# Kernel tuning notes

Measured on AMD Instinct MI355X. Metric: run time of the kernel, lower is better.

Reference implementation:

```python
import jax, jax.numpy as jnp
import numpy as np

B, S, E = 256, 500, 128
NUM_Q, NUM_C, DL = 10000, 1000, 100


def _linear_params(key, fan_in, fan_out):
    kw, kb = jax.random.split(key)
    W = jax.random.normal(kw, (fan_out, fan_in), jnp.float32) * 0.02
    b = jnp.zeros((fan_out,), jnp.float32)
    return W, b


def setup_inputs() -> dict:
    key = jax.random.key(0)
    ks = jax.random.split(key, 24)
    W1, b1 = _linear_params(ks[0], 4 * E, E)
    W2, b2 = _linear_params(ks[1], E, E)
    W3, b3 = _linear_params(ks[2], E, E)
    W4, b4 = _linear_params(ks[3], 2 * E, E)
    W5, b5 = _linear_params(ks[4], 2 * E, E)
    W6, b6 = _linear_params(ks[5], 4 * E, E)
    inp = {
        'q': jax.random.randint(ks[6], (B, S), 0, NUM_Q + 1, dtype=jnp.int32),
        'c': jax.random.randint(ks[7], (B, S), 0, NUM_C + 1, dtype=jnp.int32),
        'sd': jax.random.randint(ks[8], (B, S), 0, DL + 2, dtype=jnp.int32),
        'qd': jax.random.randint(ks[9], (B, S), 0, DL + 2, dtype=jnp.int32),
        'a': jax.random.randint(ks[10], (B, S), 0, 2, dtype=jnp.int32),
        'qshft': jax.random.randint(ks[11], (B, S), 0, NUM_Q + 1, dtype=jnp.int32),
        'cshft': jax.random.randint(ks[12], (B, S), 0, NUM_C + 1, dtype=jnp.int32),
        'sdshft': jax.random.randint(ks[13], (B, S), 0, DL + 2, dtype=jnp.int32),
        'qdshft': jax.random.randint(ks[14], (B, S), 0, DL + 2, dtype=jnp.int32),
        'q_embedding': jax.random.normal(ks[15], (B, S, E), jnp.float32),
        'c_tab': jax.random.normal(ks[16], (NUM_C + 1, E), jnp.float32) * 0.02,
        'sd_tab': jax.random.normal(ks[17], (DL + 2, E), jnp.float32) * 0.02,
        'qd_tab': jax.random.normal(ks[18], (DL + 2, E), jnp.float32) * 0.02,
        'a_tab': jax.random.normal(ks[19], (2, E), jnp.float32) * 0.02,
        'knowledge': jax.random.normal(ks[20], (1, E), jnp.float32) * 0.1,
        'W1': W1, 'b1': b1, 'W2': W2, 'b2': b2, 'W3': W3, 'b3': b3,
        'W4': W4, 'b4': b4, 'W5': W5, 'b5': b5, 'W6': W6, 'b6': b6,
    }
    return inp


def reference(q, c, sd, qd, a, qshft, cshft, sdshft, qdshft, q_embedding,
              c_tab, sd_tab, qd_tab, a_tab, knowledge,
              W1, b1, W2, b2, W3, b3, W4, b4, W5, b5, W6, b6):
    # padding_idx=0 embeddings -> zero row 0
    mask0 = lambda t: t.at[0].set(0.0)
    c_e = mask0(c_tab)[c]      # [B,S,E]
    sd_e = mask0(sd_tab)[sd]   # [B,S,E]
    qd_e = mask0(qd_tab)[qd]   # [B,S,E]
    a_e = a_tab[a]             # [B,S,E]
    # linear_1 on concatenated (q, c, sd, qd) embeddings
    input_data = jnp.concatenate([q_embedding, c_e, sd_e, qd_e], -1) @ W1.T + b1  # [B,S,E]
    # time-major for scan
    xs = (jnp.swapaxes(input_data, 0, 1), jnp.swapaxes(a_e, 0, 1),
          jnp.swapaxes(sd_e, 0, 1), jnp.swapaxes(qd_e, 0, 1))
    k0 = jnp.broadcast_to(knowledge, (q.shape[0], knowledge.shape[1]))  # [B,E]

    def step(k, x):
        inp_t, a_t, sd_t, qd_t = x
        qq = k - inp_t
        g_sdf = jax.nn.sigmoid(qq @ W2.T + b2)
        sdft = g_sdf * jnp.tanh(qq @ W3.T + b3)      # dropout in eval mode = identity
        xcat = jnp.concatenate([sdft, a_t], -1)
        g_pka = jax.nn.sigmoid(xcat @ W4.T + b4)
        pkat = g_pka * jnp.tanh(xcat @ W5.T + b5)
        ins = jnp.concatenate([k, a_t, sd_t, qd_t], -1)
        g_ksu = jax.nn.sigmoid(ins @ W6.T + b6)
        k_new = g_ksu * k + (1.0 - g_ksu) * pkat
        return k_new, None

    k_final, _ = jax.lax.scan(step, k0, xs)
    return jax.nn.sigmoid(k_final)  # [B,E]
```

## Files before the change

kernel.cpp:

```cpp
#include <hip/hip_runtime.h>

typedef unsigned short u16;
typedef unsigned int u32;
typedef short bf16x8 __attribute__((ext_vector_type(8)));
typedef float f32x4 __attribute__((ext_vector_type(4)));

#define S_LEN 500
#define NB 256
#define EDIM 128

__device__ __forceinline__ float bf2f(u16 u) { return __uint_as_float(((u32)u) << 16); }
__device__ __forceinline__ u16 f2bf(float f) {
    u32 x = __float_as_uint(f);
    x += 0x7FFFu + ((x >> 16) & 1u);
    return (u16)(x >> 16);
}
__device__ __forceinline__ u32 cvtpk(float lo, float hi) {
    u32 r;
    asm("v_cvt_pk_bf16_f32 %0, %1, %2" : "=v"(r) : "v"(lo), "v"(hi));
    return r;
}
__device__ __forceinline__ float fexp(float x) { return __builtin_amdgcn_exp2f(x * 1.44269504089f); }
__device__ __forceinline__ float frcp(float x) { return __builtin_amdgcn_rcpf(x); }
__device__ __forceinline__ float sigm(float x) { return frcp(1.0f + fexp(-x)); }
__device__ __forceinline__ float tanh_(float x) { return 1.0f - 2.0f * frcp(1.0f + fexp(2.0f * x)); }
__device__ __forceinline__ int iclamp(int v, int hi) { return v < 0 ? 0 : (v > hi ? hi : v); }

__device__ __forceinline__ void wgsync(volatile int* c, int target) {
    __asm__ volatile("s_waitcnt lgkmcnt(0)" ::: "memory");
    if ((threadIdx.x & 63) == 0) atomicAdd((int*)c, 1);
    while (*c < target) {}
    __asm__ volatile("" ::: "memory");
}

__device__ __forceinline__ bool detect_bf16(const void* q) {
    const u16* w = (const u16*)q;
    int plaus = 0;
#pragma unroll 1
    for (int i = 0; i < 64; ++i) {
        const u16 v = w[2 * i];
        const int e = (v >> 7) & 0xFF;
        plaus += (v == 0 || (e >= 100 && e <= 130)) ? 1 : 0;
    }
    return plaus >= 48;
}
__device__ __forceinline__ float ldF(const void* p, int i, bool bf) {
    return bf ? bf2f(((const u16*)p)[i]) : ((const float*)p)[i];
}
template <bool BF>
__device__ __forceinline__ bf16x8 ldfragT(const void* p, int i) {
    if (BF) return *(const bf16x8*)((const u16*)p + i);
    const float* f = (const float*)p + i;
    bf16x8 r;
#pragma unroll
    for (int e = 0; e < 8; ++e) r[e] = (short)f2bf(f[e]);
    return r;
}
__device__ __forceinline__ bf16x8 ldfragR(const void* p, int i, bool bf) {
    if (bf) return *(const bf16x8*)((const u16*)p + i);
    const float* f = (const float*)p + i;
    bf16x8 r;
#pragma unroll
    for (int e = 0; e < 8; ++e) r[e] = (short)f2bf(f[e]);
    return r;
}

__global__ void dimkt_sentinel(u16* __restrict__ out, u16 val) {
    out[blockIdx.x * 256 + threadIdx.x] = val;
}

__global__ void dimkt_qe16(const float* __restrict__ qf, u16* __restrict__ qe16) {
    if (detect_bf16(qf)) return;
    const int i = (blockIdx.x * 256 + threadIdx.x) * 8;
    const float4 a = *(const float4*)(qf + i);
    const float4 b = *(const float4*)(qf + i + 4);
    ushort4 lo, hi;
    lo.x = f2bf(a.x); lo.y = f2bf(a.y); lo.z = f2bf(a.z); lo.w = f2bf(a.w);
    hi.x = f2bf(b.x); hi.y = f2bf(b.y); hi.z = f2bf(b.z); hi.w = f2bf(b.w);
    *(ushort4*)(qe16 + i) = lo;
    *(ushort4*)(qe16 + i + 4) = hi;
}

__global__ void dimkt_w1bf(const void* __restrict__ W1, const void* __restrict__ qref,
                           u16* __restrict__ W1b) {
    const bool bf = detect_bf16(qref);
    const int i = blockIdx.x * 256 + threadIdx.x;
    W1b[i] = bf ? ((const u16*)W1)[i] : f2bf(((const float*)W1)[i]);
}

__global__ void dimkt_tabs(const void* __restrict__ q_emb,
                           const void* __restrict__ c_tab, const void* __restrict__ sd_tab,
                           const void* __restrict__ qd_tab, const void* __restrict__ a_tab,
                           const void* __restrict__ W1, const void* __restrict__ W4,
                           const void* __restrict__ W5, const void* __restrict__ W6,
                           const void* __restrict__ b4, const void* __restrict__ b5,
                           const void* __restrict__ b6,
                           float* __restrict__ cW1p, float* __restrict__ sdQ,
                           float* __restrict__ qdQ, float* __restrict__ aW6p,
                           float* __restrict__ c4t, float* __restrict__ c5t) {
    const bool bf = detect_bf16(q_emb);
    __shared__ float src[128];
    const int r = blockIdx.x, n = threadIdx.x;
    const void* srcp; const void* W; const void* bias = nullptr;
    int soff, koff, ld, oidx; float* outp; bool mask;
    if (r < 1001)      { srcp = c_tab;  soff = r * 128;               W = W1; koff = 128; ld = 512; outp = cW1p; oidx = r * 128 + n;           mask = (r == 0); }
    else if (r < 1103) { int rr = r - 1001; srcp = sd_tab; soff = rr * 128; W = W1; koff = 256; ld = 512; outp = sdQ;  oidx = rr * 256 + n * 2;     mask = (rr == 0); }
    else if (r < 1205) { int rr = r - 1103; srcp = qd_tab; soff = rr * 128; W = W1; koff = 384; ld = 512; outp = qdQ;  oidx = rr * 256 + n * 2;     mask = (rr == 0); }
    else if (r < 1307) { int rr = r - 1205; srcp = sd_tab; soff = rr * 128; W = W6; koff = 256; ld = 512; outp = sdQ;  oidx = rr * 256 + n * 2 + 1; mask = (rr == 0); }
    else if (r < 1409) { int rr = r - 1307; srcp = qd_tab; soff = rr * 128; W = W6; koff = 384; ld = 512; outp = qdQ;  oidx = rr * 256 + n * 2 + 1; mask = (rr == 0); }
    else if (r < 1411) { int rr = r - 1409; srcp = a_tab;  soff = rr * 128; W = W6; koff = 128; ld = 512; outp = aW6p; oidx = rr * 128 + n;         bias = b6; mask = false; }
    else if (r < 1413) { int rr = r - 1411; srcp = a_tab;  soff = rr * 128; W = W4; koff = 128; ld = 256; outp = c4t;  oidx = rr * 128 + n;         bias = b4; mask = false; }
    else               { int rr = r - 1413; srcp = a_tab;  soff = rr * 128; W = W5; koff = 128; ld = 256; outp = c5t;  oidx = rr * 128 + n;         bias = b5; mask = false; }
    src[n] = ldF(srcp, soff + n, bf);
    __syncthreads();
    float acc = 0.f;
    if (!mask) {
        if (bf) {
            const u16* Wp = (const u16*)W + n * ld + koff;
#pragma unroll 4
            for (int k = 0; k < 128; k += 8) {
                const ushort4 wa = *(const ushort4*)(Wp + k);
                const ushort4 wb = *(const ushort4*)(Wp + k + 4);
                acc += src[k] * bf2f(wa.x) + src[k + 1] * bf2f(wa.y)
                     + src[k + 2] * bf2f(wa.z) + src[k + 3] * bf2f(wa.w)
                     + src[k + 4] * bf2f(wb.x) + src[k + 5] * bf2f(wb.y)
                     + src[k + 6] * bf2f(wb.z) + src[k + 7] * bf2f(wb.w);
            }
        } else {
            const float* Wp = (const float*)W + n * ld + koff;
#pragma unroll 4
            for (int k = 0; k < 128; k += 4) {
                const float4 w4 = *(const float4*)(Wp + k);
                acc += src[k] * w4.x + src[k + 1] * w4.y + src[k + 2] * w4.z + src[k + 3] * w4.w;
            }
        }
        if (bias) acc += ldF(bias, n, bf);
    }
    outp[oidx] = acc;
}

__global__ void dimkt_inp(const void* __restrict__ q_emb, const u16* __restrict__ qe16,
                          const u16* __restrict__ W1b, const int fastpath,
                          const void* __restrict__ W1, const void* __restrict__ b1,
                          const int* __restrict__ cI, const int* __restrict__ sI,
                          const int* __restrict__ qI, const int* __restrict__ aI,
                          const float* __restrict__ cW1p, const float* __restrict__ sdQ,
                          const float* __restrict__ qdQ, const float* __restrict__ aW6p,
                          u16* __restrict__ INP16, u32* __restrict__ INPZ6T, const int pk) {
    const bool bf = detect_bf16(q_emb);
    const int t = blockIdx.x, rc = blockIdx.y;
    const int lane = threadIdx.x, quad = lane >> 4, l15 = lane & 15;
    const bool fA = bf || (fastpath != 0);
    const u16* aes = bf ? (const u16*)q_emb : qe16;
    bf16x8 ae[4];
#pragma unroll
    for (int ks = 0; ks < 4; ++ks) {
        const int off = ((rc * 16 + l15) * S_LEN + t) * EDIM + ks * 32 + quad * 8;
        ae[ks] = fA ? *(const bf16x8*)(aes + off) : ldfragR(q_emb, off, false);
    }
    int cx[4], sx[4], qx[4], ax[4];
#pragma unroll
    for (int i = 0; i < 4; ++i) {
        const int off = (rc * 16 + quad * 4 + i) * S_LEN + t;
        cx[i] = iclamp(cI[off], 1000);
        sx[i] = iclamp(sI[off], 101);
        qx[i] = iclamp(qI[off], 101);
        ax[i] = iclamp(aI[off], 1);
    }
#pragma unroll 1
    for (int ct = 0; ct < 8; ++ct) {
        const int colc = ct * 16 + l15;
        bf16x8 w[4];
#pragma unroll
        for (int ks = 0; ks < 4; ++ks) {
            const int woff = colc * 512 + ks * 32 + quad * 8;
            w[ks] = fastpath ? *(const bf16x8*)(W1b + woff) : ldfragR(W1, woff, bf);
        }
        const float b1c = ldF(b1, colc, bf);
        f32x4 acc; float z6v[4];
#pragma unroll
        for (int i = 0; i < 4; ++i) {
            const float2 sgp = *(const float2*)(sdQ + sx[i] * 256 + colc * 2);
            const float2 qgp = *(const float2*)(qdQ + qx[i] * 256 + colc * 2);
            acc[i] = b1c + cW1p[cx[i] * 128 + colc] + sgp.x + qgp.x;
            z6v[i] = pk ? (aW6p[ax[i] * 128 + colc] + sgp.y + qgp.y) : 0.f;
        }
#pragma unroll
        for (int ks = 0; ks < 4; ++ks)
            acc = __builtin_amdgcn_mfma_f32_16x16x32_bf16(ae[ks], w[ks], acc, 0, 0, 0);
        if (pk) {
            uint4 st;
            st.x = cvtpk(acc[0], z6v[0]); st.y = cvtpk(acc[1], z6v[1]);
            st.z = cvtpk(acc[2], z6v[2]); st.w = cvtpk(acc[3], z6v[3]);
            *(uint4*)(INPZ6T + ((size_t)t * 128 + colc) * 256 + rc * 16 + quad * 4) = st;
        } else {
#pragma unroll
            for (int i = 0; i < 4; ++i)
                INP16[((size_t)t * 256 + rc * 16 + quad * 4 + i) * 128 + colc] = f2bf(acc[i]);
        }
    }
}

template <bool BF>
__global__ __launch_bounds__(512, 2) void dimkt_scan_pk(
    const void* __restrict__ q_emb, const u32* __restrict__ INPZ6T,
    const int* __restrict__ aI,
    const void* __restrict__ W2, const void* __restrict__ b2,
    const void* __restrict__ W3, const void* __restrict__ b3,
    const void* __restrict__ W4, const void* __restrict__ W5,
    const void* __restrict__ W6, const void* __restrict__ knowledge,
    const float* __restrict__ c4t, const float* __restrict__ c5t,
    void* __restrict__ outv) {
    if (detect_bf16(q_emb) != BF) return;
    __shared__ __align__(16) u16 kbuf[16][136];
    __shared__ __align__(16) u16 qqbuf[16][136];
    __shared__ __align__(16) u16 sdbuf[16][136];
    __shared__ int sctr;

    const int tid = threadIdx.x;
    const int wv = tid >> 6, lane = tid & 63;
    const int quad = lane >> 4, l15 = lane & 15;
    const int b0 = blockIdx.x * 16;
    const int col = wv * 16 + l15;

    bf16x8 fW2[4], fW3[4], fW4[4], fW5[4], fW6[4];
#pragma unroll
    for (int ks = 0; ks < 4; ++ks) {
        const int ko = ks * 32 + quad * 8;
        fW2[ks] = ldfragT<BF>(W2, col * 128 + ko);
        fW3[ks] = ldfragT<BF>(W3, col * 128 + ko);
        fW4[ks] = ldfragT<BF>(W4, col * 256 + ko);
        fW5[ks] = ldfragT<BF>(W5, col * 256 + ko);
        fW6[ks] = ldfragT<BF>(W6, col * 512 + ko);
    }
    const float b2v = ldF(b2, col, BF);
    const float b3v = ldF(b3, col, BF);
    const float c4_0 = c4t[col], c4_1 = c4t[128 + col];
    const float c5_0 = c5t[col], c5_1 = c5t[128 + col];

    const u32* pzBase = INPZ6T + (size_t)col * 256 + b0 + quad * 4;
    const int aRow = (b0 + quad * 4) * S_LEN;

    float kold[4], z6c[4], g[4];
    int ac[4];
    {
        const float k0 = ldF(knowledge, col, BF);
        const u16 k0b = f2bf(k0);
        const uint4 pz0 = *(const uint4*)pzBase;
        const u32 pzv[4] = {pz0.x, pz0.y, pz0.z, pz0.w};
        if (tid == 0) sctr = 0;
#pragma unroll
        for (int i = 0; i < 4; ++i) {
            ac[i] = iclamp(aI[aRow + i * S_LEN], 1);
            z6c[i] = __uint_as_float(pzv[i] & 0xFFFF0000u);
            const float inp0 = __uint_as_float(pzv[i] << 16);
            kold[i] = k0;
            kbuf[quad * 4 + i][col] = k0b;
            qqbuf[quad * 4 + i][col] = f2bf(k0 - inp0);
        }
    }
    __syncthreads();

    int bar = 0;
#pragma unroll 1
    for (int t = 0; t < S_LEN; ++t) {
        const int tp = (t + 1 < S_LEN) ? t + 1 : S_LEN - 1;
        int an[4];
#pragma unroll
        for (int i = 0; i < 4; ++i) an[i] = iclamp(aI[aRow + i * S_LEN + tp], 1);
        const uint4 pzN = *(const uint4*)(pzBase + (size_t)tp * 32768);

        bf16x8 aq[4], ak[4];
#pragma unroll
        for (int ks = 0; ks < 4; ++ks) {
            aq[ks] = *(const bf16x8*)&qqbuf[l15][ks * 32 + quad * 8];
            ak[ks] = *(const bf16x8*)&kbuf[l15][ks * 32 + quad * 8];
        }
        f32x4 Y2a = (f32x4){b2v, b2v, b2v, b2v}, Y2b = (f32x4){0.f, 0.f, 0.f, 0.f};
        f32x4 Y3a = (f32x4){b3v, b3v, b3v, b3v}, Y3b = (f32x4){0.f, 0.f, 0.f, 0.f};
        f32x4 Y6a = (f32x4){z6c[0], z6c[1], z6c[2], z6c[3]}, Y6b = (f32x4){0.f, 0.f, 0.f, 0.f};
        Y2a = __builtin_amdgcn_mfma_f32_16x16x32_bf16(aq[0], fW2[0], Y2a, 0, 0, 0);
        Y3a = __builtin_amdgcn_mfma_f32_16x16x32_bf16(aq[0], fW3[0], Y3a, 0, 0, 0);
        Y6a = __builtin_amdgcn_mfma_f32_16x16x32_bf16(ak[0], fW6[0], Y6a, 0, 0, 0);
        Y2b = __builtin_amdgcn_mfma_f32_16x16x32_bf16(aq[2], fW2[2], Y2b, 0, 0, 0);
        Y3b = __builtin_amdgcn_mfma_f32_16x16x32_bf16(aq[2], fW3[2], Y3b, 0, 0, 0);
        Y6b = __builtin_amdgcn_mfma_f32_16x16x32_bf16(ak[2], fW6[2], Y6b, 0, 0, 0);
        Y2a = __builtin_amdgcn_mfma_f32_16x16x32_bf16(aq[1], fW2[1], Y2a, 0, 0, 0);
        Y3a = __builtin_amdgcn_mfma_f32_16x16x32_bf16(aq[1], fW3[1], Y3a, 0, 0, 0);
        Y6a = __builtin_amdgcn_mfma_f32_16x16x32_bf16(ak[1], fW6[1], Y6a, 0, 0, 0);
        Y2b = __builtin_amdgcn_mfma_f32_16x16x32_bf16(aq[3], fW2[3], Y2b, 0, 0, 0);
        Y3b = __builtin_amdgcn_mfma_f32_16x16x32_bf16(aq[3], fW3[3], Y3b, 0, 0, 0);
        Y6b = __builtin_amdgcn_mfma_f32_16x16x32_bf16(ak[3], fW6[3], Y6b, 0, 0, 0);
        const f32x4 Y2 = Y2a + Y2b, Y3 = Y3a + Y3b, Y6 = Y6a + Y6b;
        float sdv[4];
#pragma unroll
        for (int i = 0; i < 4; ++i) sdv[i] = sigm(Y2[i]) * tanh_(Y3[i]);
        {
            const u32 s01 = cvtpk(sdv[0], sdv[1]), s23 = cvtpk(sdv[2], sdv[3]);
            sdbuf[quad * 4 + 0][col] = (u16)s01;
            sdbuf[quad * 4 + 1][col] = (u16)(s01 >> 16);
            sdbuf[quad * 4 + 2][col] = (u16)s23;
            sdbuf[quad * 4 + 3][col] = (u16)(s23 >> 16);
        }
        bar += 8; wgsync(&sctr, bar);

        bf16x8 as[4];
#pragma unroll
        for (int ks = 0; ks < 4; ++ks)
            as[ks] = *(const bf16x8*)&sdbuf[l15][ks * 32 + quad * 8];
#pragma unroll
        for (int i = 0; i < 4; ++i) g[i] = sigm(Y6[i]);
        f32x4 Y4a = (f32x4){ac[0] ? c4_1 : c4_0, ac[1] ? c4_1 : c4_0,
                            ac[2] ? c4_1 : c4_0, ac[3] ? c4_1 : c4_0};
        f32x4 Y5a = (f32x4){ac[0] ? c5_1 : c5_0, ac[1] ? c5_1 : c5_0,
                            ac[2] ? c5_1 : c5_0, ac[3] ? c5_1 : c5_0};
        f32x4 Y4b = (f32x4){0.f, 0.f, 0.f, 0.f}, Y5b = (f32x4){0.f, 0.f, 0.f, 0.f};
        Y4a = __builtin_amdgcn_mfma_f32_16x16x32_bf16(as[0], fW4[0], Y4a, 0, 0, 0);
        Y5a = __builtin_amdgcn_mfma_f32_16x16x32_bf16(as[0], fW5[0], Y5a, 0, 0, 0);
        Y4b = __builtin_amdgcn_mfma_f32_16x16x32_bf16(as[2], fW4[2], Y4b, 0, 0, 0);
        Y5b = __builtin_amdgcn_mfma_f32_16x16x32_bf16(as[2], fW5[2], Y5b, 0, 0, 0);
        Y4a = __builtin_amdgcn_mfma_f32_16x16x32_bf16(as[1], fW4[1], Y4a, 0, 0, 0);
        Y5a = __builtin_amdgcn_mfma_f32_16x16x32_bf16(as[1], fW5[1], Y5a, 0, 0, 0);
        Y4b = __builtin_amdgcn_mfma_f32_16x16x32_bf16(as[3], fW4[3], Y4b, 0, 0, 0);
        Y5b = __builtin_amdgcn_mfma_f32_16x16x32_bf16(as[3], fW5[3], Y5b, 0, 0, 0);
        const f32x4 Y4 = Y4a + Y4b, Y5 = Y5a + Y5b;
        const u32 pzv[4] = {pzN.x, pzN.y, pzN.z, pzN.w};
        float knA[4], qqA[4];
#pragma unroll
        for (int i = 0; i < 4; ++i) {
            const float pk = sigm(Y4[i]) * tanh_(Y5[i]);
            const float kn = g[i] * kold[i] + (1.0f - g[i]) * pk;
            kold[i] = kn; knA[i] = kn;
            qqA[i] = kn - __uint_as_float(pzv[i] << 16);
        }
        {
            const u32 k01 = cvtpk(knA[0], knA[1]), k23 = cvtpk(knA[2], knA[3]);
            const u32 q01 = cvtpk(qqA[0], qqA[1]), q23 = cvtpk(qqA[2], qqA[3]);
            kbuf[quad * 4 + 0][col] = (u16)k01;
            kbuf[quad * 4 + 1][col] = (u16)(k01 >> 16);
            kbuf[quad * 4 + 2][col] = (u16)k23;
            kbuf[quad * 4 + 3][col] = (u16)(k23 >> 16);
            qqbuf[quad * 4 + 0][col] = (u16)q01;
            qqbuf[quad * 4 + 1][col] = (u16)(q01 >> 16);
            qqbuf[quad * 4 + 2][col] = (u16)q23;
            qqbuf[quad * 4 + 3][col] = (u16)(q23 >> 16);
        }
#pragma unroll
        for (int i = 0; i < 4; ++i) {
            z6c[i] = __uint_as_float(pzv[i] & 0xFFFF0000u);
            ac[i] = an[i];
        }
        bar += 8; wgsync(&sctr, bar);
    }

#pragma unroll
    for (int i = 0; i < 4; ++i) {
        const int row = quad * 4 + i;
        const float v = sigm(kold[i]);
        const int off = (b0 + row) * EDIM + col;
        if (BF) ((u16*)outv)[off] = f2bf(v);
        else    ((float*)outv)[off] = v;
    }
}

template <bool BF>
__global__ __launch_bounds__(512, 2) void dimkt_scan_fb(
    const void* __restrict__ q_emb, const u16* __restrict__ INP16,
    const int* __restrict__ cI, const int* __restrict__ sI,
    const int* __restrict__ qI, const int* __restrict__ aI,
    const void* __restrict__ W2, const void* __restrict__ b2,
    const void* __restrict__ W3, const void* __restrict__ b3,
    const void* __restrict__ W4, const void* __restrict__ W5,
    const void* __restrict__ W6, const void* __restrict__ knowledge,
    const float* __restrict__ sdQ, const float* __restrict__ qdQ,
    const float* __restrict__ aW6p, const float* __restrict__ c4t,
    const float* __restrict__ c5t, void* __restrict__ outv) {
    if (detect_bf16(q_emb) != BF) return;
    __shared__ __align__(16) u16 kbuf[16][136];
    __shared__ __align__(16) u16 qqbuf[16][136];
    __shared__ __align__(16) u16 sdbuf[16][136];
    __shared__ u32 idxL[16][S_LEN];
    __shared__ int sctr;
    extern __shared__ __align__(16) u16 dynLDS[];
    u16* sdT = dynLDS;
    u16* qdT = dynLDS + 102 * 130;
    float* aW6L = (float*)(dynLDS + 2 * 102 * 130);

    const int tid = threadIdx.x;
    const int wv = tid >> 6, lane = tid & 63;
    const int quad = lane >> 4, l15 = lane & 15;
    const int b0 = blockIdx.x * 16;
    const int col = wv * 16 + l15;
    const int col2 = col * 2;

    bf16x8 fW2[4], fW3[4], fW4[4], fW5[4], fW6[4];
#pragma unroll
    for (int ks = 0; ks < 4; ++ks) {
        const int ko = ks * 32 + quad * 8;
        fW2[ks] = ldfragT<BF>(W2, col * 128 + ko);
        fW3[ks] = ldfragT<BF>(W3, col * 128 + ko);
        fW4[ks] = ldfragT<BF>(W4, col * 256 + ko);
        fW5[ks] = ldfragT<BF>(W5, col * 256 + ko);
        fW6[ks] = ldfragT<BF>(W6, col * 512 + ko);
    }
    const float b2v = ldF(b2, col, BF);
    const float b3v = ldF(b3, col, BF);
    const float c4_0 = c4t[col], c4_1 = c4t[128 + col];
    const float c5_0 = c5t[col], c5_1 = c5t[128 + col];

#pragma unroll 1
    for (int r = 0; r < 16; ++r)
#pragma unroll 1
        for (int t = tid; t < S_LEN; t += 512) {
            const int off = (b0 + r) * S_LEN + t;
            idxL[r][t] = (u32)iclamp(cI[off], 1000)
                       | ((u32)iclamp(sI[off], 101) << 10)
                       | ((u32)iclamp(qI[off], 101) << 17)
                       | ((u32)iclamp(aI[off], 1) << 24);
        }
#pragma unroll 1
    for (int v = tid; v < 102 * 128; v += 512) {
        const int sx = v >> 7, cc = v & 127;
        sdT[sx * 130 + cc] = f2bf(sdQ[sx * 256 + cc * 2 + 1]);
        qdT[sx * 130 + cc] = f2bf(qdQ[sx * 256 + cc * 2 + 1]);
    }
    if (tid < 256) {
        const int rr = tid >> 7, cc = tid & 127;
        aW6L[rr * 132 + cc] = aW6p[rr * 128 + cc];
    }
    if (tid == 0) sctr = 0;
    __syncthreads();

    float kold[4], z6c[4], g[4];
    int ac[4];
    {
        const float k0 = ldF(knowledge, col, BF);
        const u16 k0b = f2bf(k0);
#pragma unroll
        for (int i = 0; i < 4; ++i) {
            const u32 p = idxL[quad * 4 + i][0];
            const int sx = (p >> 10) & 127, qx = (p >> 17) & 127, ax = (p >> 24) & 1;
            ac[i] = ax;
            const float2 sgp = *(const float2*)(sdQ + sx * 256 + col2);
            const float2 qgp = *(const float2*)(qdQ + qx * 256 + col2);
            z6c[i] = aW6p[ax * 128 + col] + sgp.y + qgp.y;
            const float inp0 = bf2f(INP16[(size_t)(b0 + quad * 4 + i) * 128 + col]);
            kold[i] = k0;
            kbuf[quad * 4 + i][col] = k0b;
            qqbuf[quad * 4 + i][col] = f2bf(k0 - inp0);
        }
    }
    u32 pk4[4];
#pragma unroll
    for (int i = 0; i < 4; ++i) pk4[i] = idxL[quad * 4 + i][1];
    __syncthreads();

    int bar = 0;
#pragma unroll 1
    for (int t = 0; t < S_LEN; ++t) {
        const int tf2 = (t + 2 < S_LEN) ? t + 2 : S_LEN - 1;
        const int tp = (t + 1 < S_LEN) ? t + 1 : S_LEN - 1;
        int an[4];
        u16 inpN[4];
        float sw6[4], qw6[4], agv[4];
#pragma unroll
        for (int i = 0; i < 4; ++i) {
            const u32 p = pk4[i];
            const int sx = (p >> 10) & 127, qx = (p >> 17) & 127;
            an[i] = (p >> 24) & 1;
            inpN[i] = INP16[((size_t)tp * 256 + b0 + quad * 4 + i) * 128 + col];
            sw6[i] = bf2f(sdT[sx * 130 + col]);
            qw6[i] = bf2f(qdT[qx * 130 + col]);
            agv[i] = aW6L[an[i] * 132 + col];
        }
#pragma unroll
        for (int i = 0; i < 4; ++i) pk4[i] = idxL[quad * 4 + i][tf2];

        bf16x8 aq[4], ak[4];
#pragma unroll
        for (int ks = 0; ks < 4; ++ks) {
            aq[ks] = *(const bf16x8*)&qqbuf[l15][ks * 32 + quad * 8];
            ak[ks] = *(const bf16x8*)&kbuf[l15][ks * 32 + quad * 8];
        }
        f32x4 Y2a = (f32x4){b2v, b2v, b2v, b2v}, Y2b = (f32x4){0.f, 0.f, 0.f, 0.f};
        f32x4 Y3a = (f32x4){b3v, b3v, b3v, b3v}, Y3b = (f32x4){0.f, 0.f, 0.f, 0.f};
        f32x4 Y6a = (f32x4){z6c[0], z6c[1], z6c[2], z6c[3]}, Y6b = (f32x4){0.f, 0.f, 0.f, 0.f};
        Y2a = __builtin_amdgcn_mfma_f32_16x16x32_bf16(aq[0], fW2[0], Y2a, 0, 0, 0);
        Y3a = __builtin_amdgcn_mfma_f32_16x16x32_bf16(aq[0], fW3[0], Y3a, 0, 0, 0);
        Y6a = __builtin_amdgcn_mfma_f32_16x16x32_bf16(ak[0], fW6[0], Y6a, 0, 0, 0);
        Y2b = __builtin_amdgcn_mfma_f32_16x16x32_bf16(aq[2], fW2[2], Y2b, 0, 0, 0);
        Y3b = __builtin_amdgcn_mfma_f32_16x16x32_bf16(aq[2], fW3[2], Y3b, 0, 0, 0);
        Y6b = __builtin_amdgcn_mfma_f32_16x16x32_bf16(ak[2], fW6[2], Y6b, 0, 0, 0);
        Y2a = __builtin_amdgcn_mfma_f32_16x16x32_bf16(aq[1], fW2[1], Y2a, 0, 0, 0);
        Y3a = __builtin_amdgcn_mfma_f32_16x16x32_bf16(aq[1], fW3[1], Y3a, 0, 0, 0);
        Y6a = __builtin_amdgcn_mfma_f32_16x16x32_bf16(ak[1], fW6[1], Y6a, 0, 0, 0);
        Y2b = __builtin_amdgcn_mfma_f32_16x16x32_bf16(aq[3], fW2[3], Y2b, 0, 0, 0);
        Y3b = __builtin_amdgcn_mfma_f32_16x16x32_bf16(aq[3], fW3[3], Y3b, 0, 0, 0);
        Y6b = __builtin_amdgcn_mfma_f32_16x16x32_bf16(ak[3], fW6[3], Y6b, 0, 0, 0);
        const f32x4 Y2 = Y2a + Y2b, Y3 = Y3a + Y3b, Y6 = Y6a + Y6b;
        float sdv[4];
#pragma unroll
        for (int i = 0; i < 4; ++i) sdv[i] = sigm(Y2[i]) * tanh_(Y3[i]);
        {
            const u32 s01 = cvtpk(sdv[0], sdv[1]), s23 = cvtpk(sdv[2], sdv[3]);
            sdbuf[quad * 4 + 0][col] = (u16)s01;
            sdbuf[quad * 4 + 1][col] = (u16)(s01 >> 16);
            sdbuf[quad * 4 + 2][col] = (u16)s23;
            sdbuf[quad * 4 + 3][col] = (u16)(s23 >> 16);
        }
        bar += 8; wgsync(&sctr, bar);

        bf16x8 as[4];
#pragma unroll
        for (int ks = 0; ks < 4; ++ks)
            as[ks] = *(const bf16x8*)&sdbuf[l15][ks * 32 + quad * 8];
#pragma unroll
        for (int i = 0; i < 4; ++i) g[i] = sigm(Y6[i]);
        f32x4 Y4a = (f32x4){ac[0] ? c4_1 : c4_0, ac[1] ? c4_1 : c4_0,
                            ac[2] ? c4_1 : c4_0, ac[3] ? c4_1 : c4_0};
        f32x4 Y5a = (f32x4){ac[0] ? c5_1 : c5_0, ac[1] ? c5_1 : c5_0,
                            ac[2] ? c5_1 : c5_0, ac[3] ? c5_1 : c5_0};
        f32x4 Y4b = (f32x4){0.f, 0.f, 0.f, 0.f}, Y5b = (f32x4){0.f, 0.f, 0.f, 0.f};
        Y4a = __builtin_amdgcn_mfma_f32_16x16x32_bf16(as[0], fW4[0], Y4a, 0, 0, 0);
        Y5a = __builtin_amdgcn_mfma_f32_16x16x32_bf16(as[0], fW5[0], Y5a, 0, 0, 0);
        Y4b = __builtin_amdgcn_mfma_f32_16x16x32_bf16(as[2], fW4[2], Y4b, 0, 0, 0);
        Y5b = __builtin_amdgcn_mfma_f32_16x16x32_bf16(as[2], fW5[2], Y5b, 0, 0, 0);
        Y4a = __builtin_amdgcn_mfma_f32_16x16x32_bf16(as[1], fW4[1], Y4a, 0, 0, 0);
        Y5a = __builtin_amdgcn_mfma_f32_16x16x32_bf16(as[1], fW5[1], Y5a, 0, 0, 0);
        Y4b = __builtin_amdgcn_mfma_f32_16x16x32_bf16(as[3], fW4[3], Y4b, 0, 0, 0);
        Y5b = __builtin_amdgcn_mfma_f32_16x16x32_bf16(as[3], fW5[3], Y5b, 0, 0, 0);
        const f32x4 Y4 = Y4a + Y4b, Y5 = Y5a + Y5b;
        float knA[4], qqA[4];
#pragma unroll
        for (int i = 0; i < 4; ++i) {
            const float pk = sigm(Y4[i]) * tanh_(Y5[i]);
            const float kn = g[i] * kold[i] + (1.0f - g[i]) * pk;
            kold[i] = kn; knA[i] = kn;
            qqA[i] = kn - bf2f(inpN[i]);
        }
        {
            const u32 k01 = cvtpk(knA[0], knA[1]), k23 = cvtpk(knA[2], knA[3]);
            const u32 q01 = cvtpk(qqA[0], qqA[1]), q23 = cvtpk(qqA[2], qqA[3]);
            kbuf[quad * 4 + 0][col] = (u16)k01;
            kbuf[quad * 4 + 1][col] = (u16)(k01 >> 16);
            kbuf[quad * 4 + 2][col] = (u16)k23;
            kbuf[quad * 4 + 3][col] = (u16)(k23 >> 16);
            qqbuf[quad * 4 + 0][col] = (u16)q01;
            qqbuf[quad * 4 + 1][col] = (u16)(q01 >> 16);
            qqbuf[quad * 4 + 2][col] = (u16)q23;
            qqbuf[quad * 4 + 3][col] = (u16)(q23 >> 16);
        }
#pragma unroll
        for (int i = 0; i < 4; ++i) {
            z6c[i] = agv[i] + sw6[i] + qw6[i];
            ac[i] = an[i];
        }
        bar += 8; wgsync(&sctr, bar);
    }

#pragma unroll
    for (int i = 0; i < 4; ++i) {
        const int row = quad * 4 + i;
        const float v = sigm(kold[i]);
        const int off = (b0 + row) * EDIM + col;
        if (BF) ((u16*)outv)[off] = f2bf(v);
        else    ((float*)outv)[off] = v;
    }
}

extern "C" void kernel_launch(void* const* d_in, const int* in_sizes, int n_in,
                              void* d_out, int out_size, void* d_ws, size_t ws_size,
                              hipStream_t stream) {
    static const int exp_sizes[27] = {
        128000, 128000, 128000, 128000, 128000,
        128000, 128000, 128000, 128000,
        16384000,
        128128, 13056, 13056, 256, 128,
        65536, 128, 16384, 128, 16384, 128,
        32768, 128, 32768, 128, 65536, 128
    };
    bool sizes_ok = (n_in == 27) && (out_size == 32768);
    if (sizes_ok)
        for (int i = 0; i < 27; ++i)
            if (in_sizes[i] != exp_sizes[i]) { sizes_ok = false; break; }
    if (!sizes_ok) {
        dimkt_sentinel<<<dim3(128), dim3(256), 0, stream>>>((u16*)d_out, (u16)0xC080);
        return;
    }
    const size_t WS_NEED = 724480;
    const size_t WS_FB   = WS_NEED + 32768000u;
    if (ws_size < WS_FB) {
        dimkt_sentinel<<<dim3(128), dim3(256), 0, stream>>>((u16*)d_out, (u16)0x4110);
        return;
    }
    const size_t WS_PK   = WS_NEED + 65536000u;
    const size_t WS_FAST = WS_PK + 32768000u + 131072u;
    const int pk   = (ws_size >= WS_PK) ? 1 : 0;
    const int fast = (ws_size >= WS_FAST) ? 1 : 0;

    const int* c   = (const int*)d_in[1];
    const int* sd  = (const int*)d_in[2];
    const int* qd  = (const int*)d_in[3];
    const int* a   = (const int*)d_in[4];
    const void* q_emb = d_in[9];
    const void* c_tab = d_in[10];
    const void* sd_tab = d_in[11];
    const void* qd_tab = d_in[12];
    const void* a_tab = d_in[13];
    const void* knowledge = d_in[14];
    const void* W1 = d_in[15]; const void* b1 = d_in[16];
    const void* W2 = d_in[17]; const void* b2 = d_in[18];
    const void* W3 = d_in[19]; const void* b3 = d_in[20];
    const void* W4 = d_in[21]; const void* b4 = d_in[22];
    const void* W5 = d_in[23]; const void* b5 = d_in[24];
    const void* W6 = d_in[25]; const void* b6 = d_in[26];

    float* wsf = (float*)d_ws;
    float* cW1p = wsf;
    float* sdQ  = wsf + 128128;
    float* qdQ  = wsf + 154240;
    float* aW6p = wsf + 180352;
    float* c4t  = wsf + 180608;
    float* c5t  = wsf + 180864;
    u16* INP16  = (u16*)((char*)d_ws + WS_NEED);
    u32* INPZ6T = (u32*)((char*)d_ws + WS_NEED);
    u16* qe16   = (u16*)((char*)d_ws + WS_PK);
    u16* W1b    = (u16*)((char*)d_ws + WS_PK + 32768000u);

    dimkt_tabs<<<dim3(1415), dim3(128), 0, stream>>>(
        q_emb, c_tab, sd_tab, qd_tab, a_tab, W1, W4, W5, W6, b4, b5, b6,
        cW1p, sdQ, qdQ, aW6p, c4t, c5t);

    if (fast) {
        dimkt_qe16<<<dim3(8000), dim3(256), 0, stream>>>((const float*)q_emb, qe16);
        dimkt_w1bf<<<dim3(256), dim3(256), 0, stream>>>(W1, q_emb, W1b);
    }

    dimkt_inp<<<dim3(500, 16), dim3(64), 0, stream>>>(
        q_emb, qe16, W1b, fast, W1, b1, c, sd, qd, a,
        cW1p, sdQ, qdQ, aW6p, INP16, INPZ6T, pk);

    if (pk) {
        dimkt_scan_pk<true><<<dim3(16), dim3(512), 0, stream>>>(
            q_emb, INPZ6T, a, W2, b2, W3, b3, W4, W5, W6, knowledge, c4t, c5t, d_out);
        dimkt_scan_pk<false><<<dim3(16), dim3(512), 0, stream>>>(
            q_emb, INPZ6T, a, W2, b2, W3, b3, W4, W5, W6, knowledge, c4t, c5t, d_out);
    } else {
        constexpr int DYN_BYTES = 2 * 102 * 130 * 2 + 2 * 132 * 4;
        hipFuncSetAttribute(reinterpret_cast<const void*>(&dimkt_scan_fb<true>),
                            hipFuncAttributeMaxDynamicSharedMemorySize, DYN_BYTES);
        hipFuncSetAttribute(reinterpret_cast<const void*>(&dimkt_scan_fb<false>),
                            hipFuncAttributeMaxDynamicSharedMemorySize, DYN_BYTES);
        dimkt_scan_fb<true><<<dim3(16), dim3(512), DYN_BYTES, stream>>>(
            q_emb, INP16, c, sd, qd, a, W2, b2, W3, b3, W4, W5, W6, knowledge,
            sdQ, qdQ, aW6p, c4t, c5t, d_out);
        dimkt_scan_fb<false><<<dim3(16), dim3(512), DYN_BYTES, stream>>>(
            q_emb, INP16, c, sd, qd, a, W2, b2, W3, b3, W4, W5, W6, knowledge,
            sdQ, qdQ, aW6p, c4t, c5t, d_out);
    }
}
```

Before: 998.3 us.

## XOR-swizzle LDS state buffers, single-chain MFMA accumulation, peel last scan step

Applies an XOR swizzle to the column index when writing and reading the k, qq and sd LDS buffers to avoid bank conflicts on the fragment loads. It also replaces the split a/b MFMA accumulator chains with a single serial chain per output, removing the final vector adds but lengthening dependency chains. The last time step is peeled out of the loop, which removes the clamped prefetch index, and loads switch to incremented pointers.

```diff
diff --git a/kernel.cpp b/kernel.cpp
--- a/kernel.cpp
+++ b/kernel.cpp
@@ -222,6 +222,8 @@
     const int quad = lane >> 4, l15 = lane & 15;
     const int b0 = blockIdx.x * 16;
     const int col = wv * 16 + l15;
+    const int quadX = quad ^ (l15 >> 2);
+    const int wcolX = col ^ (quad << 3);
 
     bf16x8 fW2[4], fW3[4], fW4[4], fW5[4], fW6[4];
 #pragma unroll
@@ -239,7 +241,7 @@
     const float c5_0 = c5t[col], c5_1 = c5t[128 + col];
 
     const u32* pzBase = INPZ6T + (size_t)col * 256 + b0 + quad * 4;
-    const int aRow = (b0 + quad * 4) * S_LEN;
+    const int* aBase = aI + (b0 + quad * 4) * S_LEN;
 
     float kold[4], z6c[4], g[4];
     int ac[4];
@@ -251,79 +253,69 @@
         if (tid == 0) sctr = 0;
 #pragma unroll
         for (int i = 0; i < 4; ++i) {
-            ac[i] = iclamp(aI[aRow + i * S_LEN], 1);
+            ac[i] = iclamp(aBase[i * S_LEN], 1);
             z6c[i] = __uint_as_float(pzv[i] & 0xFFFF0000u);
             const float inp0 = __uint_as_float(pzv[i] << 16);
             kold[i] = k0;
-            kbuf[quad * 4 + i][col] = k0b;
-            qqbuf[quad * 4 + i][col] = f2bf(k0 - inp0);
+            kbuf[quad * 4 + i][wcolX] = k0b;
+            qqbuf[quad * 4 + i][wcolX] = f2bf(k0 - inp0);
         }
     }
     __syncthreads();
 
+    const u32* pzP = pzBase + 32768;
+    const int* aP = aBase + 1;
     int bar = 0;
 #pragma unroll 1
-    for (int t = 0; t < S_LEN; ++t) {
-        const int tp = (t + 1 < S_LEN) ? t + 1 : S_LEN - 1;
+    for (int t = 0; t < S_LEN - 1; ++t) {
         int an[4];
 #pragma unroll
-        for (int i = 0; i < 4; ++i) an[i] = iclamp(aI[aRow + i * S_LEN + tp], 1);
-        const uint4 pzN = *(const uint4*)(pzBase + (size_t)tp * 32768);
+        for (int i = 0; i < 4; ++i) an[i] = iclamp(aP[i * S_LEN], 1);
+        const uint4 pzN = *(const uint4*)pzP;
+        aP += 1; pzP += 32768;
 
         bf16x8 aq[4], ak[4];
 #pragma unroll
         for (int ks = 0; ks < 4; ++ks) {
-            aq[ks] = *(const bf16x8*)&qqbuf[l15][ks * 32 + quad * 8];
-            ak[ks] = *(const bf16x8*)&kbuf[l15][ks * 32 + quad * 8];
-        }
-        f32x4 Y2a = (f32x4){b2v, b2v, b2v, b2v}, Y2b = (f32x4){0.f, 0.f, 0.f, 0.f};
-        f32x4 Y3a = (f32x4){b3v, b3v, b3v, b3v}, Y3b = (f32x4){0.f, 0.f, 0.f, 0.f};
-        f32x4 Y6a = (f32x4){z6c[0], z6c[1], z6c[2], z6c[3]}, Y6b = (f32x4){0.f, 0.f, 0.f, 0.f};
-        Y2a = __builtin_amdgcn_mfma_f32_16x16x32_bf16(aq[0], fW2[0], Y2a, 0, 0, 0);
-        Y3a = __builtin_amdgcn_mfma_f32_16x16x32_bf16(aq[0], fW3[0], Y3a, 0, 0, 0);
-        Y6a = __builtin_amdgcn_mfma_f32_16x16x32_bf16(ak[0], fW6[0], Y6a, 0, 0, 0);
-        Y2b = __builtin_amdgcn_mfma_f32_16x16x32_bf16(aq[2], fW2[2], Y2b, 0, 0, 0);
-        Y3b = __builtin_amdgcn_mfma_f32_16x16x32_bf16(aq[2], fW3[2], Y3b, 0, 0, 0);
-        Y6b = __builtin_amdgcn_mfma_f32_16x16x32_bf16(ak[2], fW6[2], Y6b, 0, 0, 0);
-        Y2a = __builtin_amdgcn_mfma_f32_16x16x32_bf16(aq[1], fW2[1], Y2a, 0, 0, 0);
-        Y3a = __builtin_amdgcn_mfma_f32_16x16x32_bf16(aq[1], fW3[1], Y3a, 0, 0, 0);
-        Y6a = __builtin_amdgcn_mfma_f32_16x16x32_bf16(ak[1], fW6[1], Y6a, 0, 0, 0);
-        Y2b = __builtin_amdgcn_mfma_f32_16x16x32_bf16(aq[3], fW2[3], Y2b, 0, 0, 0);
-        Y3b = __builtin_amdgcn_mfma_f32_16x16x32_bf16(aq[3], fW3[3], Y3b, 0, 0, 0);
-        Y6b = __builtin_amdgcn_mfma_f32_16x16x32_bf16(ak[3], fW6[3], Y6b, 0, 0, 0);
-        const f32x4 Y2 = Y2a + Y2b, Y3 = Y3a + Y3b, Y6 = Y6a + Y6b;
+            aq[ks] = *(const bf16x8*)&qqbuf[l15][ks * 32 + quadX * 8];
+            ak[ks] = *(const bf16x8*)&kbuf[l15][ks * 32 + quadX * 8];
+        }
+        f32x4 Y2 = (f32x4){b2v, b2v, b2v, b2v};
+        f32x4 Y3 = (f32x4){b3v, b3v, b3v, b3v};
+        f32x4 Y6 = (f32x4){z6c[0], z6c[1], z6c[2], z6c[3]};
+#pragma unroll
+        for (int ks = 0; ks < 4; ++ks) {
+            Y2 = __builtin_amdgcn_mfma_f32_16x16x32_bf16(aq[ks], fW2[ks], Y2, 0, 0, 0);
+            Y3 = __builtin_amdgcn_mfma_f32_16x16x32_bf16(aq[ks], fW3[ks], Y3, 0, 0, 0);
+            Y6 = __builtin_amdgcn_mfma_f32_16x16x32_bf16(ak[ks], fW6[ks], Y6, 0, 0, 0);
+        }
         float sdv[4];
 #pragma unroll
         for (int i = 0; i < 4; ++i) sdv[i] = sigm(Y2[i]) * tanh_(Y3[i]);
         {
             const u32 s01 = cvtpk(sdv[0], sdv[1]), s23 = cvtpk(sdv[2], sdv[3]);
-            sdbuf[quad * 4 + 0][col] = (u16)s01;
-            sdbuf[quad * 4 + 1][col] = (u16)(s01 >> 16);
-            sdbuf[quad * 4 + 2][col] = (u16)s23;
-            sdbuf[quad * 4 + 3][col] = (u16)(s23 >> 16);
+            sdbuf[quad * 4 + 0][wcolX] = (u16)s01;
+            sdbuf[quad * 4 + 1][wcolX] = (u16)(s01 >> 16);
+            sdbuf[quad * 4 + 2][wcolX] = (u16)s23;
+            sdbuf[quad * 4 + 3][wcolX] = (u16)(s23 >> 16);
         }
         bar += 8; wgsync(&sctr, bar);
 
         bf16x8 as[4];
 #pragma unroll
         for (int ks = 0; ks < 4; ++ks)
-            as[ks] = *(const bf16x8*)&sdbuf[l15][ks * 32 + quad * 8];
+            as[ks] = *(const bf16x8*)&sdbuf[l15][ks * 32 + quadX * 8];
 #pragma unroll
         for (int i = 0; i < 4; ++i) g[i] = sigm(Y6[i]);
-        f32x4 Y4a = (f32x4){ac[0] ? c4_1 : c4_0, ac[1] ? c4_1 : c4_0,
-                            ac[2] ? c4_1 : c4_0, ac[3] ? c4_1 : c4_0};
-        f32x4 Y5a = (f32x4){ac[0] ? c5_1 : c5_0, ac[1] ? c5_1 : c5_0,
-                            ac[2] ? c5_1 : c5_0, ac[3] ? c5_1 : c5_0};
-        f32x4 Y4b = (f32x4){0.f, 0.f, 0.f, 0.f}, Y5b = (f32x4){0.f, 0.f, 0.f, 0.f};
-        Y4a = __builtin_amdgcn_mfma_f32_16x16x32_bf16(as[0], fW4[0], Y4a, 0, 0, 0);
-        Y5a = __builtin_amdgcn_mfma_f32_16x16x32_bf16(as[0], fW5[0], Y5a, 0, 0, 0);
-        Y4b = __builtin_amdgcn_mfma_f32_16x16x32_bf16(as[2], fW4[2], Y4b, 0, 0, 0);
-        Y5b = __builtin_amdgcn_mfma_f32_16x16x32_bf16(as[2], fW5[2], Y5b, 0, 0, 0);
-        Y4a = __builtin_amdgcn_mfma_f32_16x16x32_bf16(as[1], fW4[1], Y4a, 0, 0, 0);
-        Y5a = __builtin_amdgcn_mfma_f32_16x16x32_bf16(as[1], fW5[1], Y5a, 0, 0, 0);
-        Y4b = __builtin_amdgcn_mfma_f32_16x16x32_bf16(as[3], fW4[3], Y4b, 0, 0, 0);
-        Y5b = __builtin_amdgcn_mfma_f32_16x16x32_bf16(as[3], fW5[3], Y5b, 0, 0, 0);
-        const f32x4 Y4 = Y4a + Y4b, Y5 = Y5a + Y5b;
+        f32x4 Y4 = (f32x4){ac[0] ? c4_1 : c4_0, ac[1] ? c4_1 : c4_0,
+                           ac[2] ? c4_1 : c4_0, ac[3] ? c4_1 : c4_0};
+        f32x4 Y5 = (f32x4){ac[0] ? c5_1 : c5_0, ac[1] ? c5_1 : c5_0,
+                           ac[2] ? c5_1 : c5_0, ac[3] ? c5_1 : c5_0};
+#pragma unroll
+        for (int ks = 0; ks < 4; ++ks) {
+            Y4 = __builtin_amdgcn_mfma_f32_16x16x32_bf16(as[ks], fW4[ks], Y4, 0, 0, 0);
+            Y5 = __builtin_amdgcn_mfma_f32_16x16x32_bf16(as[ks], fW5[ks], Y5, 0, 0, 0);
+        }
         const u32 pzv[4] = {pzN.x, pzN.y, pzN.z, pzN.w};
         float knA[4], qqA[4];
 #pragma unroll
@@ -336,14 +328,14 @@
         {
             const u32 k01 = cvtpk(knA[0], knA[1]), k23 = cvtpk(knA[2], knA[3]);
             const u32 q01 = cvtpk(qqA[0], qqA[1]), q23 = cvtpk(qqA[2], qqA[3]);
-            kbuf[quad * 4 + 0][col] = (u16)k01;
-            kbuf[quad * 4 + 1][col] = (u16)(k01 >> 16);
-            kbuf[quad * 4 + 2][col] = (u16)k23;
-            kbuf[quad * 4 + 3][col] = (u16)(k23 >> 16);
-            qqbuf[quad * 4 + 0][col] = (u16)q01;
-            qqbuf[quad * 4 + 1][col] = (u16)(q01 >> 16);
-            qqbuf[quad * 4 + 2][col] = (u16)q23;
-            qqbuf[quad * 4 + 3][col] = (u16)(q23 >> 16);
+            kbuf[quad * 4 + 0][wcolX] = (u16)k01;
+            kbuf[quad * 4 + 1][wcolX] = (u16)(k01 >> 16);
+            kbuf[quad * 4 + 2][wcolX] = (u16)k23;
+            kbuf[quad * 4 + 3][wcolX] = (u16)(k23 >> 16);
+            qqbuf[quad * 4 + 0][wcolX] = (u16)q01;
+            qqbuf[quad * 4 + 1][wcolX] = (u16)(q01 >> 16);
+            qqbuf[quad * 4 + 2][wcolX] = (u16)q23;
+            qqbuf[quad * 4 + 3][wcolX] = (u16)(q23 >> 16);
         }
 #pragma unroll
         for (int i = 0; i < 4; ++i) {
@@ -351,6 +343,56 @@
             ac[i] = an[i];
         }
         bar += 8; wgsync(&sctr, bar);
+    }
+
+    {
+        bf16x8 aq[4], ak[4];
+#pragma unroll
+        for (int ks = 0; ks < 4; ++ks) {
+            aq[ks] = *(const bf16x8*)&qqbuf[l15][ks * 32 + quadX * 8];
+            ak[ks] = *(const bf16x8*)&kbuf[l15][ks * 32 + quadX * 8];
+        }
+        f32x4 Y2 = (f32x4){b2v, b2v, b2v, b2v};
+        f32x4 Y3 = (f32x4){b3v, b3v, b3v, b3v};
+        f32x4 Y6 = (f32x4){z6c[0], z6c[1], z6c[2], z6c[3]};
+#pragma unroll
+        for (int ks = 0; ks < 4; ++ks) {
+            Y2 = __builtin_amdgcn_mfma_f32_16x16x32_bf16(aq[ks], fW2[ks], Y2, 0, 0, 0);
+            Y3 = __builtin_amdgcn_mfma_f32_16x16x32_bf16(aq[ks], fW3[ks], Y3, 0, 0, 0);
+            Y6 = __builtin_amdgcn_mfma_f32_16x16x32_bf16(ak[ks], fW6[ks], Y6, 0, 0, 0);
+        }
+        float sdv[4];
+#pragma unroll
+        for (int i = 0; i < 4; ++i) sdv[i] = sigm(Y2[i]) * tanh_(Y3[i]);
+        {
+            const u32 s01 = cvtpk(sdv[0], sdv[1]), s23 = cvtpk(sdv[2], sdv[3]);
+            sdbuf[quad * 4 + 0][wcolX] = (u16)s01;
+            sdbuf[quad * 4 + 1][wcolX] = (u16)(s01 >> 16);
+            sdbuf[quad * 4 + 2][wcolX] = (u16)s23;
+            sdbuf[quad * 4 + 3][wcolX] = (u16)(s23 >> 16);
+        }
+        bar += 8; wgsync(&sctr, bar);
+
+        bf16x8 as[4];
+#pragma unroll
+        for (int ks = 0; ks < 4; ++ks)
+            as[ks] = *(const bf16x8*)&sdbuf[l15][ks * 32 + quadX * 8];
+#pragma unroll
+        for (int i = 0; i < 4; ++i) g[i] = sigm(Y6[i]);
+        f32x4 Y4 = (f32x4){ac[0] ? c4_1 : c4_0, ac[1] ? c4_1 : c4_0,
+                           ac[2] ? c4_1 : c4_0, ac[3] ? c4_1 : c4_0};
+        f32x4 Y5 = (f32x4){ac[0] ? c5_1 : c5_0, ac[1] ? c5_1 : c5_0,
+                           ac[2] ? c5_1 : c5_0, ac[3] ? c5_1 : c5_0};
+#pragma unroll
+        for (int ks = 0; ks < 4; ++ks) {
+            Y4 = __builtin_amdgcn_mfma_f32_16x16x32_bf16(as[ks], fW4[ks], Y4, 0, 0, 0);
+            Y5 = __builtin_amdgcn_mfma_f32_16x16x32_bf16(as[ks], fW5[ks], Y5, 0, 0, 0);
+        }
+#pragma unroll
+        for (int i = 0; i < 4; ++i) {
+            const float pk = sigm(Y4[i]) * tanh_(Y5[i]);
+            kold[i] = g[i] * kold[i] + (1.0f - g[i]) * pk;
+        }
     }
 
 #pragma unroll
```

After: 950.7 us. 4.8% less time.
